# Performance work log

Measured on AMD Instinct MI355X. Metric: run time of the kernel, lower is better.

The kernel has to match this reference:

```python
import jax, jax.numpy as jnp
import numpy as np
import math

B, SEQ, H, HKV, D = 2, 2048, 32, 8, 128
BLOCK, LOCAL_BLOCKS, VERT_STRIDE = 64, 16, 8
NB = SEQ // BLOCK


def _build_layout():
    # local + vertical-strided causal block-sparse layout (homo heads),
    # converted from CSR to a padded [NB, max_nnz] column-index table.
    q_idx = np.arange(NB)[:, None]
    k_idx = np.arange(NB)[None, :]
    dense = (k_idx <= q_idx) & ((q_idx - k_idx < LOCAL_BLOCKS) | ((k_idx + 1) % VERT_STRIDE == 0))
    max_nnz = int(dense.sum(1).max())  # == 18 for NB=32, local=16, stride=8
    cols = np.zeros((NB, max_nnz), np.int32)
    valid = np.zeros((NB, max_nnz), np.bool_)
    for i in range(NB):
        c = np.nonzero(dense[i])[0]
        cols[i, :c.size] = c
        valid[i, :c.size] = True
    return jnp.asarray(cols), jnp.asarray(valid)


def setup_inputs() -> dict:
    key = jax.random.key(0)
    kq, kk, kv = jax.random.split(key, 3)
    q = jax.random.normal(kq, (B, SEQ, H, D), jnp.float32)
    k = jax.random.normal(kk, (B, SEQ, HKV, D), jnp.float32)
    v = jax.random.normal(kv, (B, SEQ, HKV, D), jnp.float32)
    layout_cols, layout_mask = _build_layout()
    return {"q": q, "k": k, "v": v, "layout_cols": layout_cols, "layout_mask": layout_mask}


def _attn(q, k, v, layout_cols, layout_mask):
    Bn, S, Hq, Dh = q.shape
    Hkv = k.shape[2]
    g = Hq // Hkv               # GQA group size (q_k_ratio)
    nb, nnz = layout_cols.shape
    blk = S // nb               # block_size
    sm_scale = 1.0 / math.sqrt(Dh)
    # reshape to blocks; keep KV at Hkv heads (no repeat) and group q heads
    qb = q.reshape(Bn, nb, blk, Hkv, g, Dh).transpose(0, 3, 4, 1, 2, 5)  # [B,Hkv,g,nb,blk,D]
    kb = k.reshape(Bn, nb, blk, Hkv, Dh).transpose(0, 3, 1, 2, 4)        # [B,Hkv,nb,blk,D]
    vb = v.reshape(Bn, nb, blk, Hkv, Dh).transpose(0, 3, 1, 2, 4)
    # gather only the attended K/V blocks per query block (honors block sparsity)
    kg = jnp.take(kb, layout_cols, axis=2)  # [B,Hkv,nb,nnz,blk,D]
    vg = jnp.take(vb, layout_cols, axis=2)
    scores = jnp.einsum('bhgqmd,bhqknd->bhgqmkn', qb, kg) * sm_scale  # [B,Hkv,g,nb,blk,nnz,blk]
    # token-level causal mask + padded-column mask (past_len = 0 for prefill)
    q_tok = jnp.arange(nb)[:, None] * blk + jnp.arange(blk)[None, :]            # [nb,blk]
    k_tok = layout_cols[:, :, None] * blk + jnp.arange(blk)[None, None, :]      # [nb,nnz,blk]
    valid = layout_mask[:, None, :, None] & (k_tok[:, None] <= q_tok[:, :, None, None])  # [nb,blk,nnz,blk]
    scores = jnp.where(valid[None, None, None], scores, -jnp.inf)
    p = jax.nn.softmax(scores.reshape(Bn, Hkv, g, nb, blk, nnz * blk), axis=-1).reshape(scores.shape)
    out = jnp.einsum('bhgqmkn,bhqknd->bhgqmd', p, vg)
    return out.transpose(0, 3, 4, 1, 2, 5).reshape(Bn, S, Hq, Dh)


def reference(q, k, v, layout_cols, layout_mask):
    return _attn(q, k, v, layout_cols, layout_mask)
```

## Files before the change

kernel.cpp:

```cpp
#include <hip/hip_runtime.h>

#define B_    2
#define SEQ_  2048
#define H_    32
#define HKV_  8
#define D_    128
#define BLK_  64
#define NB_   32
#define LOCAL_ 16
#define VERT_  8

#define KSTR 136
#define VSTR 72
#define PSTR 72
#define NTASK 512

typedef __attribute__((ext_vector_type(8))) short bf16x8;
typedef __attribute__((ext_vector_type(4))) float f32x4;

__device__ __forceinline__ unsigned short f2bf(float f) {
    union { float f; unsigned u; } x; x.f = f;
    unsigned u = x.u;
    return (unsigned short)((u + 0x7FFFu + ((u >> 16) & 1u)) >> 16);
}

__global__ __launch_bounds__(512, 2)
void sparse_attn_kernel(const float* __restrict__ qg, const float* __restrict__ kg,
                        const float* __restrict__ vg, float* __restrict__ outg,
                        unsigned* __restrict__ ctr) {
    __shared__ __align__(16) unsigned short Klds[BLK_ * KSTR];
    __shared__ __align__(16) unsigned short Vlds[D_ * VSTR];
    __shared__ __align__(16) unsigned short Plds[8 * 2 * 16 * PSTR];
    __shared__ unsigned taskLds;

    const int tid  = threadIdx.x;
    const int wave = tid >> 6;
    const int lane = tid & 63;
    const int l15  = lane & 15;
    const int quad = lane >> 4;

    const float c2 = 0.12751649736230723f;
    const short oneb = (short)0x3F80;
    const bf16x8 ones = {oneb, oneb, oneb, oneb, oneb, oneb, oneb, oneb};

    for (;;) {
        __syncthreads();
        if (tid == 0) taskLds = atomicAdd(ctr, 1u);
        __syncthreads();
        const unsigned t = taskLds;
        if (t >= NTASK) break;

        const int qb   = 31 - (int)(t >> 4);
        const int bh   = (int)(t & 15);
        const int b    = bh >> 3;
        const int hkv  = bh & 7;
        const int head = hkv * 4 + (wave >> 1);
        const int rhalf = (wave & 1) * 32;

        bf16x8 qf[2][4];
#pragma unroll
        for (int rt = 0; rt < 2; ++rt) {
            const int row = qb * BLK_ + rhalf + rt * 16 + l15;
            const float* qp = qg + ((size_t)(b * SEQ_ + row) * H_ + head) * D_;
#pragma unroll
            for (int s = 0; s < 4; ++s) {
                const int d0 = s * 32 + quad * 8;
                float4 a = *(const float4*)(qp + d0);
                float4 c = *(const float4*)(qp + d0 + 4);
                bf16x8 f;
                f[0] = f2bf(a.x); f[1] = f2bf(a.y); f[2] = f2bf(a.z); f[3] = f2bf(a.w);
                f[4] = f2bf(c.x); f[5] = f2bf(c.y); f[6] = f2bf(c.z); f[7] = f2bf(c.w);
                qf[rt][s] = f;
            }
        }

        float m_i[2][4];
        f32x4 lacc[2];
        f32x4 o_acc[2][8];
#pragma unroll
        for (int rt = 0; rt < 2; ++rt) {
#pragma unroll
            for (int r = 0; r < 4; ++r) m_i[rt][r] = -INFINITY;
            lacc[rt] = f32x4{0.f, 0.f, 0.f, 0.f};
#pragma unroll
            for (int t8 = 0; t8 < 8; ++t8) o_acc[rt][t8] = f32x4{0.f, 0.f, 0.f, 0.f};
        }

        for (int j = 0; j <= qb; ++j) {
            if (!(((qb - j) < LOCAL_) || (((j + 1) & (VERT_ - 1)) == 0))) continue;

            __syncthreads();
            {
                const float* kp = kg + ((size_t)(b * SEQ_ + j * BLK_) * HKV_ + hkv) * D_;
#pragma unroll
                for (int it = 0; it < 4; ++it) {
                    const int idx = it * 512 + tid;
                    const int row = idx >> 5;
                    const int c4  = idx & 31;
                    float4 kk = *(const float4*)(kp + row * (HKV_ * D_) + c4 * 4);
                    ushort4 u;
                    u.x = f2bf(kk.x); u.y = f2bf(kk.y); u.z = f2bf(kk.z); u.w = f2bf(kk.w);
                    *(ushort4*)&Klds[row * KSTR + c4 * 4] = u;
                }
                const float* vp = vg + ((size_t)(b * SEQ_ + j * BLK_) * HKV_ + hkv) * D_;
#pragma unroll
                for (int it = 0; it < 4; ++it) {
                    const int idx = it * 512 + tid;
                    const int row = idx >> 5;
                    const int c4  = idx & 31;
                    float4 vv = *(const float4*)(vp + row * (HKV_ * D_) + c4 * 4);
                    float vals[4] = {vv.x, vv.y, vv.z, vv.w};
#pragma unroll
                    for (int i2 = 0; i2 < 4; ++i2) {
                        const int d  = c4 * 4 + i2;
                        const int p2 = (row + (((d >> 2) & 7) << 3)) & 63;
                        Vlds[d * VSTR + p2] = f2bf(vals[i2]);
                    }
                }
            }
            __syncthreads();

            f32x4 sacc[2][4];
#pragma unroll
            for (int rt = 0; rt < 2; ++rt)
#pragma unroll
                for (int t4 = 0; t4 < 4; ++t4) sacc[rt][t4] = f32x4{0.f, 0.f, 0.f, 0.f};
#pragma unroll
            for (int t4 = 0; t4 < 4; ++t4) {
#pragma unroll
                for (int s = 0; s < 4; ++s) {
                    const bf16x8 kf = *(const bf16x8*)&Klds[(t4 * 16 + l15) * KSTR + s * 32 + quad * 8];
                    sacc[0][t4] = __builtin_amdgcn_mfma_f32_16x16x32_bf16(qf[0][s], kf, sacc[0][t4], 0, 0, 0);
                    sacc[1][t4] = __builtin_amdgcn_mfma_f32_16x16x32_bf16(qf[1][s], kf, sacc[1][t4], 0, 0, 0);
                }
            }

            if (j == qb) {
#pragma unroll
                for (int rt = 0; rt < 2; ++rt) {
                    const int rowbase = rhalf + rt * 16 + quad * 4;
#pragma unroll
                    for (int t4 = 0; t4 < 4; ++t4) {
                        const int col = t4 * 16 + l15;
#pragma unroll
                        for (int r = 0; r < 4; ++r)
                            if (col > rowbase + r) sacc[rt][t4][r] = -INFINITY;
                    }
                }
            }

#pragma unroll
            for (int rt = 0; rt < 2; ++rt) {
                float alpha[4], mc[4];
#pragma unroll
                for (int r = 0; r < 4; ++r) {
                    float mx = fmaxf(fmaxf(sacc[rt][0][r], sacc[rt][1][r]),
                                     fmaxf(sacc[rt][2][r], sacc[rt][3][r]));
#pragma unroll
                    for (int off = 8; off >= 1; off >>= 1)
                        mx = fmaxf(mx, __shfl_xor(mx, off, 64));
                    const float mnew = fmaxf(m_i[rt][r], mx);
                    alpha[r] = exp2f(c2 * (m_i[rt][r] - mnew));
                    m_i[rt][r] = mnew;
                    mc[r] = c2 * mnew;
                }
                lacc[rt][0] *= alpha[0]; lacc[rt][1] *= alpha[1];
                lacc[rt][2] *= alpha[2]; lacc[rt][3] *= alpha[3];
#pragma unroll
                for (int t8 = 0; t8 < 8; ++t8)
#pragma unroll
                    for (int r = 0; r < 4; ++r) o_acc[rt][t8][r] *= alpha[r];

                unsigned short* pl = &Plds[(wave * 2 + rt) * 16 * PSTR];
#pragma unroll
                for (int t4 = 0; t4 < 4; ++t4)
#pragma unroll
                    for (int r = 0; r < 4; ++r) {
                        const float p = exp2f(fmaf(sacc[rt][t4][r], c2, -mc[r]));
                        pl[(quad * 4 + r) * PSTR + t4 * 16 + l15] = f2bf(p);
                    }
            }
            asm volatile("s_waitcnt lgkmcnt(0)" ::: "memory");

#pragma unroll
            for (int s2 = 0; s2 < 2; ++s2) {
                const bf16x8 pf0 = *(const bf16x8*)&Plds[(wave * 2 + 0) * 16 * PSTR + l15 * PSTR + s2 * 32 + quad * 8];
                const bf16x8 pf1 = *(const bf16x8*)&Plds[(wave * 2 + 1) * 16 * PSTR + l15 * PSTR + s2 * 32 + quad * 8];
                lacc[0] = __builtin_amdgcn_mfma_f32_16x16x32_bf16(pf0, ones, lacc[0], 0, 0, 0);
                lacc[1] = __builtin_amdgcn_mfma_f32_16x16x32_bf16(pf1, ones, lacc[1], 0, 0, 0);
                const int k0 = s2 * 32 + quad * 8;
#pragma unroll
                for (int t8 = 0; t8 < 8; ++t8) {
                    const int n  = t8 * 16 + l15;
                    const int p2 = (k0 + (((n >> 2) & 7) << 3)) & 63;
                    const bf16x8 vf = *(const bf16x8*)&Vlds[n * VSTR + p2];
                    o_acc[0][t8] = __builtin_amdgcn_mfma_f32_16x16x32_bf16(pf0, vf, o_acc[0][t8], 0, 0, 0);
                    o_acc[1][t8] = __builtin_amdgcn_mfma_f32_16x16x32_bf16(pf1, vf, o_acc[1][t8], 0, 0, 0);
                }
            }
        }

#pragma unroll
        for (int rt = 0; rt < 2; ++rt)
#pragma unroll
            for (int r = 0; r < 4; ++r) {
                const float inv_l = 1.0f / lacc[rt][r];
                const int row = qb * BLK_ + rhalf + rt * 16 + quad * 4 + r;
                float* op = outg + ((size_t)(b * SEQ_ + row) * H_ + head) * D_;
#pragma unroll
                for (int t8 = 0; t8 < 8; ++t8)
                    op[t8 * 16 + l15] = o_acc[rt][t8][r] * inv_l;
            }
    }
}

extern "C" void kernel_launch(void* const* d_in, const int* in_sizes, int n_in,
                              void* d_out, int out_size, void* d_ws, size_t ws_size,
                              hipStream_t stream) {
    const float* q = (const float*)d_in[0];
    const float* k = (const float*)d_in[1];
    const float* v = (const float*)d_in[2];
    float* out = (float*)d_out;
    unsigned* ctr = (unsigned*)d_ws;
    hipMemsetAsync(ctr, 0, sizeof(unsigned), stream);
    sparse_attn_kernel<<<dim3(NTASK), dim3(512), 0, stream>>>(q, k, v, out, ctr);
}
```

Measured before the change: 273.9 us.

## Use 1024-thread persistent blocks with register-prefetched K/V and lazy rescale

The block grows to 16 waves, each owning one 16-row tile of one query head, and the grid becomes 256 persistent blocks pulling tasks from an atomic counter. The K/V tile for the next valid sparse block is prefetched into registers while the current tile is computed, so global load latency overlaps the MFMA work. Float-to-bf16 conversion uses a packed conversion builtin, and the online-softmax rescale of the accumulators is skipped when no row max changed. The explicit LDS waitcnt is removed, and the single 1024-thread block per CU raises register pressure and limits occupancy.

```diff
diff --git a/kernel.cpp b/kernel.cpp
--- a/kernel.cpp
+++ b/kernel.cpp
@@ -14,6 +14,7 @@
 #define VSTR 72
 #define PSTR 72
 #define NTASK 512
+#define NBLOCK 256
 
 typedef __attribute__((ext_vector_type(8))) short bf16x8;
 typedef __attribute__((ext_vector_type(4))) float f32x4;
@@ -24,13 +25,29 @@
     return (unsigned short)((u + 0x7FFFu + ((u >> 16) & 1u)) >> 16);
 }
 
-__global__ __launch_bounds__(512, 2)
+__device__ __forceinline__ unsigned pk2(float a, float b) {
+#if defined(__has_builtin) && __has_builtin(__builtin_amdgcn_cvt_pk_bf16_f32)
+    typedef __attribute__((ext_vector_type(2))) __bf16 bf2;
+    bf2 r = __builtin_amdgcn_cvt_pk_bf16_f32(a, b);
+    unsigned u; __builtin_memcpy(&u, &r, 4); return u;
+#else
+    return (unsigned)f2bf(a) | ((unsigned)f2bf(b) << 16);
+#endif
+}
+
+__device__ __forceinline__ int next_valid(int qb, int j) {
+    for (++j; j <= qb; ++j)
+        if (((qb - j) < LOCAL_) || (((j + 1) & (VERT_ - 1)) == 0)) return j;
+    return qb + 1;
+}
+
+__global__ __launch_bounds__(1024)
 void sparse_attn_kernel(const float* __restrict__ qg, const float* __restrict__ kg,
                         const float* __restrict__ vg, float* __restrict__ outg,
                         unsigned* __restrict__ ctr) {
     __shared__ __align__(16) unsigned short Klds[BLK_ * KSTR];
     __shared__ __align__(16) unsigned short Vlds[D_ * VSTR];
-    __shared__ __align__(16) unsigned short Plds[8 * 2 * 16 * PSTR];
+    __shared__ __align__(16) unsigned short Plds[16 * 16 * PSTR];
     __shared__ unsigned taskLds;
 
     const int tid  = threadIdx.x;
@@ -38,10 +55,25 @@
     const int lane = tid & 63;
     const int l15  = lane & 15;
     const int quad = lane >> 4;
+    const int hsub = wave >> 2;
+    const int rt   = wave & 3;
+
+    const int srow0 = tid >> 5;
+    const int srow1 = srow0 + 32;
+    const int sc4   = tid & 31;
+    const int kld0  = srow0 * KSTR + sc4 * 4;
+    const int kld1  = srow1 * KSTR + sc4 * 4;
+    const int vd    = sc4 * 4;
+    const int vskew = (sc4 & 7) << 3;
+    const int vp0   = (srow0 + vskew) & 63;
+    const int vp1   = (srow1 + vskew) & 63;
+    const size_t stoff0 = (size_t)srow0 * (HKV_ * D_) + sc4 * 4;
+    const size_t stoff1 = (size_t)srow1 * (HKV_ * D_) + sc4 * 4;
 
     const float c2 = 0.12751649736230723f;
     const short oneb = (short)0x3F80;
     const bf16x8 ones = {oneb, oneb, oneb, oneb, oneb, oneb, oneb, oneb};
+    unsigned short* pl = &Plds[wave * 16 * PSTR];
 
     for (;;) {
         __syncthreads();
@@ -50,167 +82,156 @@
         const unsigned t = taskLds;
         if (t >= NTASK) break;
 
-        const int qb   = 31 - (int)(t >> 4);
-        const int bh   = (int)(t & 15);
-        const int b    = bh >> 3;
-        const int hkv  = bh & 7;
-        const int head = hkv * 4 + (wave >> 1);
-        const int rhalf = (wave & 1) * 32;
-
-        bf16x8 qf[2][4];
-#pragma unroll
-        for (int rt = 0; rt < 2; ++rt) {
-            const int row = qb * BLK_ + rhalf + rt * 16 + l15;
+        const int qb  = 31 - (int)(t >> 4);
+        const int bh  = (int)(t & 15);
+        const int b   = bh >> 3;
+        const int hkv = bh & 7;
+        const int head = hkv * 4 + hsub;
+
+        const float* kbase = kg + ((size_t)(b * SEQ_) * HKV_ + hkv) * D_;
+        const float* vbase = vg + ((size_t)(b * SEQ_) * HKV_ + hkv) * D_;
+
+        bf16x8 qf[4];
+        {
+            const int row = qb * BLK_ + rt * 16 + l15;
             const float* qp = qg + ((size_t)(b * SEQ_ + row) * H_ + head) * D_;
 #pragma unroll
             for (int s = 0; s < 4; ++s) {
-                const int d0 = s * 32 + quad * 8;
-                float4 a = *(const float4*)(qp + d0);
-                float4 c = *(const float4*)(qp + d0 + 4);
-                bf16x8 f;
-                f[0] = f2bf(a.x); f[1] = f2bf(a.y); f[2] = f2bf(a.z); f[3] = f2bf(a.w);
-                f[4] = f2bf(c.x); f[5] = f2bf(c.y); f[6] = f2bf(c.z); f[7] = f2bf(c.w);
-                qf[rt][s] = f;
-            }
-        }
-
-        float m_i[2][4];
-        f32x4 lacc[2];
-        f32x4 o_acc[2][8];
-#pragma unroll
-        for (int rt = 0; rt < 2; ++rt) {
-#pragma unroll
-            for (int r = 0; r < 4; ++r) m_i[rt][r] = -INFINITY;
-            lacc[rt] = f32x4{0.f, 0.f, 0.f, 0.f};
-#pragma unroll
-            for (int t8 = 0; t8 < 8; ++t8) o_acc[rt][t8] = f32x4{0.f, 0.f, 0.f, 0.f};
-        }
-
-        for (int j = 0; j <= qb; ++j) {
-            if (!(((qb - j) < LOCAL_) || (((j + 1) & (VERT_ - 1)) == 0))) continue;
+                const float4 a = *(const float4*)(qp + s * 32 + quad * 8);
+                const float4 c = *(const float4*)(qp + s * 32 + quad * 8 + 4);
+                uint4 u = { pk2(a.x, a.y), pk2(a.z, a.w), pk2(c.x, c.y), pk2(c.z, c.w) };
+                __builtin_memcpy(&qf[s], &u, 16);
+            }
+        }
+
+        float m_i[4];
+        f32x4 lacc = f32x4{0.f, 0.f, 0.f, 0.f};
+        f32x4 o_acc[8];
+#pragma unroll
+        for (int r = 0; r < 4; ++r) m_i[r] = -INFINITY;
+#pragma unroll
+        for (int t8 = 0; t8 < 8; ++t8) o_acc[t8] = f32x4{0.f, 0.f, 0.f, 0.f};
+
+        int j = next_valid(qb, -1);
+        float4 kpr0, kpr1, vpr0, vpr1;
+        {
+            const float* kp = kbase + (size_t)j * BLK_ * HKV_ * D_;
+            const float* vp = vbase + (size_t)j * BLK_ * HKV_ * D_;
+            kpr0 = *(const float4*)(kp + stoff0); kpr1 = *(const float4*)(kp + stoff1);
+            vpr0 = *(const float4*)(vp + stoff0); vpr1 = *(const float4*)(vp + stoff1);
+        }
+
+        while (j <= qb) {
+            const int jn = next_valid(qb, j);
 
             __syncthreads();
             {
-                const float* kp = kg + ((size_t)(b * SEQ_ + j * BLK_) * HKV_ + hkv) * D_;
-#pragma unroll
-                for (int it = 0; it < 4; ++it) {
-                    const int idx = it * 512 + tid;
-                    const int row = idx >> 5;
-                    const int c4  = idx & 31;
-                    float4 kk = *(const float4*)(kp + row * (HKV_ * D_) + c4 * 4);
-                    ushort4 u;
-                    u.x = f2bf(kk.x); u.y = f2bf(kk.y); u.z = f2bf(kk.z); u.w = f2bf(kk.w);
-                    *(ushort4*)&Klds[row * KSTR + c4 * 4] = u;
-                }
-                const float* vp = vg + ((size_t)(b * SEQ_ + j * BLK_) * HKV_ + hkv) * D_;
-#pragma unroll
-                for (int it = 0; it < 4; ++it) {
-                    const int idx = it * 512 + tid;
-                    const int row = idx >> 5;
-                    const int c4  = idx & 31;
-                    float4 vv = *(const float4*)(vp + row * (HKV_ * D_) + c4 * 4);
-                    float vals[4] = {vv.x, vv.y, vv.z, vv.w};
-#pragma unroll
-                    for (int i2 = 0; i2 < 4; ++i2) {
-                        const int d  = c4 * 4 + i2;
-                        const int p2 = (row + (((d >> 2) & 7) << 3)) & 63;
-                        Vlds[d * VSTR + p2] = f2bf(vals[i2]);
-                    }
-                }
+                uint2 u0 = { pk2(kpr0.x, kpr0.y), pk2(kpr0.z, kpr0.w) };
+                uint2 u1 = { pk2(kpr1.x, kpr1.y), pk2(kpr1.z, kpr1.w) };
+                *(uint2*)&Klds[kld0] = u0;
+                *(uint2*)&Klds[kld1] = u1;
+                unsigned a0 = pk2(vpr0.x, vpr0.y), a1 = pk2(vpr0.z, vpr0.w);
+                Vlds[(vd + 0) * VSTR + vp0] = (unsigned short)a0;
+                Vlds[(vd + 1) * VSTR + vp0] = (unsigned short)(a0 >> 16);
+                Vlds[(vd + 2) * VSTR + vp0] = (unsigned short)a1;
+                Vlds[(vd + 3) * VSTR + vp0] = (unsigned short)(a1 >> 16);
+                unsigned b0 = pk2(vpr1.x, vpr1.y), b1 = pk2(vpr1.z, vpr1.w);
+                Vlds[(vd + 0) * VSTR + vp1] = (unsigned short)b0;
+                Vlds[(vd + 1) * VSTR + vp1] = (unsigned short)(b0 >> 16);
+                Vlds[(vd + 2) * VSTR + vp1] = (unsigned short)b1;
+                Vlds[(vd + 3) * VSTR + vp1] = (unsigned short)(b1 >> 16);
             }
             __syncthreads();
 
-            f32x4 sacc[2][4];
-#pragma unroll
-            for (int rt = 0; rt < 2; ++rt)
-#pragma unroll
-                for (int t4 = 0; t4 < 4; ++t4) sacc[rt][t4] = f32x4{0.f, 0.f, 0.f, 0.f};
+            if (jn <= qb) {
+                const float* kp = kbase + (size_t)jn * BLK_ * HKV_ * D_;
+                const float* vp = vbase + (size_t)jn * BLK_ * HKV_ * D_;
+                kpr0 = *(const float4*)(kp + stoff0); kpr1 = *(const float4*)(kp + stoff1);
+                vpr0 = *(const float4*)(vp + stoff0); vpr1 = *(const float4*)(vp + stoff1);
+            }
+
+            f32x4 sacc[4];
 #pragma unroll
             for (int t4 = 0; t4 < 4; ++t4) {
+                f32x4 acc = f32x4{0.f, 0.f, 0.f, 0.f};
 #pragma unroll
                 for (int s = 0; s < 4; ++s) {
                     const bf16x8 kf = *(const bf16x8*)&Klds[(t4 * 16 + l15) * KSTR + s * 32 + quad * 8];
-                    sacc[0][t4] = __builtin_amdgcn_mfma_f32_16x16x32_bf16(qf[0][s], kf, sacc[0][t4], 0, 0, 0);
-                    sacc[1][t4] = __builtin_amdgcn_mfma_f32_16x16x32_bf16(qf[1][s], kf, sacc[1][t4], 0, 0, 0);
+                    acc = __builtin_amdgcn_mfma_f32_16x16x32_bf16(qf[s], kf, acc, 0, 0, 0);
                 }
+                sacc[t4] = acc;
             }
 
             if (j == qb) {
-#pragma unroll
-                for (int rt = 0; rt < 2; ++rt) {
-                    const int rowbase = rhalf + rt * 16 + quad * 4;
-#pragma unroll
-                    for (int t4 = 0; t4 < 4; ++t4) {
-                        const int col = t4 * 16 + l15;
-#pragma unroll
-                        for (int r = 0; r < 4; ++r)
-                            if (col > rowbase + r) sacc[rt][t4][r] = -INFINITY;
-                    }
+                const int rowbase = rt * 16 + quad * 4;
+#pragma unroll
+                for (int t4 = 0; t4 < 4; ++t4) {
+                    const int col = t4 * 16 + l15;
+#pragma unroll
+                    for (int r = 0; r < 4; ++r)
+                        if (col > rowbase + r) sacc[t4][r] = -INFINITY;
                 }
             }
 
-#pragma unroll
-            for (int rt = 0; rt < 2; ++rt) {
-                float alpha[4], mc[4];
-#pragma unroll
-                for (int r = 0; r < 4; ++r) {
-                    float mx = fmaxf(fmaxf(sacc[rt][0][r], sacc[rt][1][r]),
-                                     fmaxf(sacc[rt][2][r], sacc[rt][3][r]));
-#pragma unroll
-                    for (int off = 8; off >= 1; off >>= 1)
-                        mx = fmaxf(mx, __shfl_xor(mx, off, 64));
-                    const float mnew = fmaxf(m_i[rt][r], mx);
-                    alpha[r] = exp2f(c2 * (m_i[rt][r] - mnew));
-                    m_i[rt][r] = mnew;
-                    mc[r] = c2 * mnew;
-                }
-                lacc[rt][0] *= alpha[0]; lacc[rt][1] *= alpha[1];
-                lacc[rt][2] *= alpha[2]; lacc[rt][3] *= alpha[3];
-#pragma unroll
-                for (int t8 = 0; t8 < 8; ++t8)
-#pragma unroll
-                    for (int r = 0; r < 4; ++r) o_acc[rt][t8][r] *= alpha[r];
-
-                unsigned short* pl = &Plds[(wave * 2 + rt) * 16 * PSTR];
-#pragma unroll
-                for (int t4 = 0; t4 < 4; ++t4)
-#pragma unroll
-                    for (int r = 0; r < 4; ++r) {
-                        const float p = exp2f(fmaf(sacc[rt][t4][r], c2, -mc[r]));
-                        pl[(quad * 4 + r) * PSTR + t4 * 16 + l15] = f2bf(p);
-                    }
-            }
-            asm volatile("s_waitcnt lgkmcnt(0)" ::: "memory");
+            float alpha[4], mc[4];
+#pragma unroll
+            for (int r = 0; r < 4; ++r) {
+                float mx = fmaxf(fmaxf(sacc[0][r], sacc[1][r]), fmaxf(sacc[2][r], sacc[3][r]));
+#pragma unroll
+                for (int off = 8; off >= 1; off >>= 1)
+                    mx = fmaxf(mx, __shfl_xor(mx, off, 64));
+                const float mnew = fmaxf(m_i[r], mx);
+                alpha[r] = exp2f(c2 * (m_i[r] - mnew));
+                m_i[r] = mnew;
+                mc[r] = c2 * mnew;
+            }
+            const float amin = fminf(fminf(alpha[0], alpha[1]), fminf(alpha[2], alpha[3]));
+            if (__any(amin < 0.999999f)) {
+                const f32x4 av = {alpha[0], alpha[1], alpha[2], alpha[3]};
+                lacc *= av;
+#pragma unroll
+                for (int t8 = 0; t8 < 8; ++t8) o_acc[t8] *= av;
+            }
+
+#pragma unroll
+            for (int t4 = 0; t4 < 4; ++t4) {
+                const float p0 = exp2f(fmaf(sacc[t4][0], c2, -mc[0]));
+                const float p1 = exp2f(fmaf(sacc[t4][1], c2, -mc[1]));
+                const float p2 = exp2f(fmaf(sacc[t4][2], c2, -mc[2]));
+                const float p3 = exp2f(fmaf(sacc[t4][3], c2, -mc[3]));
+                const unsigned u01 = pk2(p0, p1), u23 = pk2(p2, p3);
+                const int cb = t4 * 16 + l15;
+                pl[(quad * 4 + 0) * PSTR + cb] = (unsigned short)u01;
+                pl[(quad * 4 + 1) * PSTR + cb] = (unsigned short)(u01 >> 16);
+                pl[(quad * 4 + 2) * PSTR + cb] = (unsigned short)u23;
+                pl[(quad * 4 + 3) * PSTR + cb] = (unsigned short)(u23 >> 16);
+            }
 
 #pragma unroll
             for (int s2 = 0; s2 < 2; ++s2) {
-                const bf16x8 pf0 = *(const bf16x8*)&Plds[(wave * 2 + 0) * 16 * PSTR + l15 * PSTR + s2 * 32 + quad * 8];
-                const bf16x8 pf1 = *(const bf16x8*)&Plds[(wave * 2 + 1) * 16 * PSTR + l15 * PSTR + s2 * 32 + quad * 8];
-                lacc[0] = __builtin_amdgcn_mfma_f32_16x16x32_bf16(pf0, ones, lacc[0], 0, 0, 0);
-                lacc[1] = __builtin_amdgcn_mfma_f32_16x16x32_bf16(pf1, ones, lacc[1], 0, 0, 0);
+                const bf16x8 pf = *(const bf16x8*)&pl[l15 * PSTR + s2 * 32 + quad * 8];
+                lacc = __builtin_amdgcn_mfma_f32_16x16x32_bf16(pf, ones, lacc, 0, 0, 0);
                 const int k0 = s2 * 32 + quad * 8;
 #pragma unroll
                 for (int t8 = 0; t8 < 8; ++t8) {
                     const int n  = t8 * 16 + l15;
                     const int p2 = (k0 + (((n >> 2) & 7) << 3)) & 63;
                     const bf16x8 vf = *(const bf16x8*)&Vlds[n * VSTR + p2];
-                    o_acc[0][t8] = __builtin_amdgcn_mfma_f32_16x16x32_bf16(pf0, vf, o_acc[0][t8], 0, 0, 0);
-                    o_acc[1][t8] = __builtin_amdgcn_mfma_f32_16x16x32_bf16(pf1, vf, o_acc[1][t8], 0, 0, 0);
+                    o_acc[t8] = __builtin_amdgcn_mfma_f32_16x16x32_bf16(pf, vf, o_acc[t8], 0, 0, 0);
                 }
             }
-        }
-
-#pragma unroll
-        for (int rt = 0; rt < 2; ++rt)
-#pragma unroll
-            for (int r = 0; r < 4; ++r) {
-                const float inv_l = 1.0f / lacc[rt][r];
-                const int row = qb * BLK_ + rhalf + rt * 16 + quad * 4 + r;
-                float* op = outg + ((size_t)(b * SEQ_ + row) * H_ + head) * D_;
-#pragma unroll
-                for (int t8 = 0; t8 < 8; ++t8)
-                    op[t8 * 16 + l15] = o_acc[rt][t8][r] * inv_l;
-            }
+            j = jn;
+        }
+
+        const int orow = qb * BLK_ + rt * 16 + quad * 4;
+#pragma unroll
+        for (int r = 0; r < 4; ++r) {
+            const float inv_l = 1.0f / lacc[r];
+            float* op = outg + ((size_t)(b * SEQ_ + orow + r) * H_ + head) * D_;
+#pragma unroll
+            for (int t8 = 0; t8 < 8; ++t8)
+                op[t8 * 16 + l15] = o_acc[t8][r] * inv_l;
+        }
     }
 }
 
@@ -223,5 +244,5 @@
     float* out = (float*)d_out;
     unsigned* ctr = (unsigned*)d_ws;
     hipMemsetAsync(ctr, 0, sizeof(unsigned), stream);
-    sparse_attn_kernel<<<dim3(NTASK), dim3(512), 0, stream>>>(q, k, v, out, ctr);
-}
+    sparse_attn_kernel<<<dim3(NBLOCK), dim3(1024), 0, stream>>>(q, k, v, out, ctr);
+}
```

After: 292.3 us. 1.07x slower.
